# Kernel tuning notes

Measured on AMD Instinct MI355X. Metric: run time of the kernel, lower is better.

## Reference

```python
import jax, jax.numpy as jnp
import numpy as np

N = 1_048_576   # number of time samples (light-curve length)
M = 8           # number of quasisep Exp kernel terms (state dimension)
LOG2PI = float(np.log(2.0 * np.pi))


def setup_inputs() -> dict:
    key = jax.random.key(0)
    k1, k2, k3, k4, k5 = jax.random.split(key, 5)
    # unsorted-but-nearly-sorted timestamps; module argsorts internally
    t = jax.random.uniform(k1, (N,), dtype=jnp.float32) * (N / 10.0)
    y = jax.random.normal(k2, (N,), dtype=jnp.float32)
    yerr = 0.1 + 0.05 * jax.random.uniform(k3, (N,), dtype=jnp.float32)
    # interleaved [log_scale_j, log_sigma_j] for M Exp terms, as ravel_pytree would produce
    log_scale = jnp.log(10.0) + 0.5 * jax.random.normal(k4, (M,), dtype=jnp.float32)
    log_sigma = 0.3 * jax.random.normal(k5, (M,), dtype=jnp.float32)
    log_kernel_param = jnp.stack([log_scale, log_sigma], axis=1).reshape(-1)
    return {"t": t, "y": y, "yerr": yerr, "log_kernel_param": log_kernel_param}


def _kalman_log_prob(ts, ys, diag, scale, sigma):
    """GP log-likelihood for k(tau)=sum_j sigma_j^2 exp(-tau/scale_j) via Kalman filter.

    State: M independent OU components; observation h = ones(M); zero mean.
    """
    Pinf = sigma * sigma                                   # stationary variances [M]
    dt = jnp.concatenate([jnp.zeros((1,), ts.dtype), jnp.diff(ts)])  # [N]

    def step(carry, inp):
        m, P, ll = carry                                   # m:[M], P:[M,M]
        dtn, yn, dn = inp
        phi = jnp.exp(-dtn / scale)                        # transition diag [M]
        m_pred = phi * m
        # P_pred = Phi P Phi^T + Q,  Q = diag(Pinf*(1-phi^2))
        P_pred = (phi[:, None] * phi[None, :]) * P + jnp.diag(Pinf * (1.0 - phi * phi))
        Ph = P_pred.sum(axis=1)                            # P_pred @ h
        S = Ph.sum() + dn                                  # innovation variance
        v = yn - m_pred.sum()                              # innovation (zero mean)
        K = Ph / S                                         # Kalman gain
        m_new = m_pred + K * v
        P_new = P_pred - K[:, None] * Ph[None, :]
        ll_new = ll - 0.5 * (LOG2PI + jnp.log(S) + v * v / S)
        return (m_new, P_new, ll_new), None

    m0 = jnp.zeros((M,), ts.dtype)
    P0 = jnp.diag(Pinf)
    (_, _, ll), _ = jax.lax.scan(step, (m0, P0, jnp.zeros((), ts.dtype)), (dt, ys, diag))
    return ll


def reference(t, y, yerr, log_kernel_param):
    # UniVarModel.log_prob: sort by time, diag = yerr^2 (has_jitter=False),
    # kernel params exponentiated, zero mean.
    inds = jnp.argsort(t)
    ts, ys, diag = t[inds], y[inds], yerr[inds] ** 2
    p = jnp.exp(log_kernel_param)
    scale, sigma = p[0::2], p[1::2]
    return _kalman_log_prob(ts, ys, diag, scale, sigma)
```

## Files before the change

### kernel.cpp

```cpp
#include <hip/hip_runtime.h>
#include <stdint.h>

typedef unsigned long long u64;

#define CHUNK 64
#define WARM  8
#define SLEN  (WARM + CHUNK)
#define CPW   8
#define PD    8
#define NB    16384
#define NR    1024
#define BCAP  128
#define HBLK  64
#define LOG2PI_F 1.8378770664093453f

__device__ __forceinline__ int bucket_of(float tv, float scale) {
    int b = (int)(tv * scale);
    return b > (NB - 1) ? (NB - 1) : (b < 0 ? 0 : b);
}

__global__ __launch_bounds__(256) void hist_k(const float4* __restrict__ t4,
                                              unsigned* __restrict__ hp,
                                              float scale, int n4) {
    __shared__ unsigned lh[NR];
    for (int v = threadIdx.x; v < NR; v += 256) lh[v] = 0u;
    __syncthreads();
    for (int i = blockIdx.x * 256 + threadIdx.x; i < n4; i += gridDim.x * 256) {
        float4 tv = t4[i];
        atomicAdd(&lh[bucket_of(tv.x, scale) >> 4], 1u);
        atomicAdd(&lh[bucket_of(tv.y, scale) >> 4], 1u);
        atomicAdd(&lh[bucket_of(tv.z, scale) >> 4], 1u);
        atomicAdd(&lh[bucket_of(tv.w, scale) >> 4], 1u);
    }
    __syncthreads();
    for (int v = threadIdx.x; v < NR; v += 256)
        hp[blockIdx.x * NR + v] = lh[v];
}

__global__ __launch_bounds__(1024) void scan_k(const unsigned* __restrict__ hp,
                                               unsigned* __restrict__ roff,
                                               unsigned* __restrict__ rcnt) {
    __shared__ unsigned ws[16];
    const int r = threadIdx.x;
    unsigned tot = 0;
#pragma unroll 8
    for (int b = 0; b < HBLK; ++b) tot += hp[b * NR + r];
    unsigned s = tot;
#pragma unroll
    for (int d = 1; d < 64; d <<= 1) {
        unsigned v = __shfl_up(s, d);
        if ((r & 63) >= d) s += v;
    }
    if ((r & 63) == 63) ws[r >> 6] = s;
    __syncthreads();
    if (r < 16) {
        unsigned v = ws[r];
#pragma unroll
        for (int d = 1; d < 16; d <<= 1) {
            unsigned x = __shfl_up(v, d);
            if (r >= d) v += x;
        }
        ws[r] = v;
    }
    __syncthreads();
    unsigned wbase = (r >= 64) ? ws[(r >> 6) - 1] : 0u;
    unsigned excl = wbase + s - tot;
    roff[r] = excl; rcnt[r] = excl;
    if (r == NR - 1) roff[NR] = excl + tot;
}

__global__ __launch_bounds__(1024) void scatter1(const float4* __restrict__ t4,
                                                 unsigned* __restrict__ rcnt,
                                                 u64* __restrict__ keys1,
                                                 float scale) {
    __shared__ unsigned lh[NR], rb[NR];
    const int tid = threadIdx.x;
    lh[tid] = 0u;
    __syncthreads();
    const int i0 = blockIdx.x * 2048 + tid;
    float4 a = t4[i0], b = t4[i0 + 1024];
    float tv[8] = {a.x, a.y, a.z, a.w, b.x, b.y, b.z, b.w};
    unsigned id0 = 4u * (unsigned)i0, id1 = 4u * (unsigned)(i0 + 1024);
    unsigned ids[8] = {id0, id0 + 1, id0 + 2, id0 + 3,
                       id1, id1 + 1, id1 + 2, id1 + 3};
    int rr[8]; unsigned lp[8];
#pragma unroll
    for (int k = 0; k < 8; ++k) {
        rr[k] = bucket_of(tv[k], scale) >> 4;
        lp[k] = atomicAdd(&lh[rr[k]], 1u);
    }
    __syncthreads();
    {
        unsigned c = lh[tid];
        rb[tid] = c ? atomicAdd(&rcnt[tid], c) : 0u;
    }
    __syncthreads();
#pragma unroll
    for (int k = 0; k < 8; ++k) {
        unsigned bits = __float_as_uint(tv[k]);
        unsigned mk = (bits & 0x80000000u) ? ~bits : (bits | 0x80000000u);
        keys1[rb[rr[k]] + lp[k]] = ((u64)mk << 32) | (u64)ids[k];
    }
}

__device__ __forceinline__ float decode_key(unsigned h) {
    unsigned b = (h & 0x80000000u) ? (h ^ 0x80000000u) : ~h;
    return __uint_as_float(b);
}

__global__ __launch_bounds__(256) void sort_k(const u64* __restrict__ keys1,
                                              const unsigned* __restrict__ roff,
                                              float* __restrict__ tS,
                                              unsigned* __restrict__ idxS,
                                              float scale) {
    __shared__ u64 sk[16 * BCAP];
    __shared__ unsigned lh[16], pre[16];
    const int r = blockIdx.x;
    const int tid = threadIdx.x;
    for (int v = tid; v < 16 * BCAP; v += 256) sk[v] = ~0ull;
    if (tid < 16) lh[tid] = 0u;
    __syncthreads();
    const unsigned s = roff[r], e = roff[r + 1];
    for (unsigned u = s + tid; u < e; u += 256) {
        u64 kk = keys1[u];
        int b16 = bucket_of(decode_key((unsigned)(kk >> 32)), scale) & 15;
        unsigned lp = atomicAdd(&lh[b16], 1u);
        if (lp < (unsigned)BCAP) sk[b16 * BCAP + lp] = kk;
    }
    __syncthreads();
    if (tid == 0) {
        unsigned acc = 0;
#pragma unroll
        for (int c = 0; c < 16; ++c) {
            pre[c] = acc;
            unsigned cc = lh[c];
            acc += (cc > (unsigned)BCAP) ? (unsigned)BCAP : cc;
        }
    }
    for (int k = 2; k <= BCAP; k <<= 1) {
        for (int j = k >> 1; j >= 1; j >>= 1) {
#pragma unroll
            for (int it = 0; it < 4; ++it) {
                int w = it * 256 + tid;
                int q = w >> 6, p = w & 63;
                int i = ((p & ~(j - 1)) << 1) | (p & (j - 1));
                int si = q * BCAP + i, sp = si + j;
                bool up = ((i & k) == 0);
                u64 a = sk[si], bb = sk[sp];
                if ((a > bb) == up) { sk[si] = bb; sk[sp] = a; }
            }
            __syncthreads();
        }
    }
#pragma unroll
    for (int cp = 0; cp < 8; ++cp) {
        int c = cp * 2 + (tid >> 7);
        int el = tid & 127;
        unsigned cc = lh[c]; cc = (cc > (unsigned)BCAP) ? (unsigned)BCAP : cc;
        if (el < (int)cc) {
            u64 kk = sk[c * BCAP + el];
            unsigned pos = s + pre[c] + el;
            tS[pos] = decode_key((unsigned)(kk >> 32));
            idxS[pos] = (unsigned)kk;
        }
    }
}

__global__ __launch_bounds__(256) void gather_pay(const uint4* __restrict__ idx4,
                                                  const float* __restrict__ src,
                                                  float* __restrict__ dst,
                                                  int squared, int n8) {
    int i = blockIdx.x * 256 + threadIdx.x;
    if (i >= n8) return;
    uint4 a = idx4[2 * i], b = idx4[2 * i + 1];
    float4 o1, o2;
    o1.x = src[a.x]; o1.y = src[a.y]; o1.z = src[a.z]; o1.w = src[a.w];
    o2.x = src[b.x]; o2.y = src[b.y]; o2.z = src[b.z]; o2.w = src[b.w];
    if (squared) {
        o1.x *= o1.x; o1.y *= o1.y; o1.z *= o1.z; o1.w *= o1.w;
        o2.x *= o2.x; o2.y *= o2.y; o2.z *= o2.z; o2.w *= o2.w;
    }
    ((float4*)dst)[2 * i] = o1;
    ((float4*)dst)[2 * i + 1] = o2;
}

#define DPPMOV(x, ctrl) __int_as_float(__builtin_amdgcn_update_dpp( \
        0, __float_as_int(x), (ctrl), 0xF, 0xF, true))
#define GSUM8(s, x) { s = (x) + DPPMOV((x), 0xB1); s += DPPMOV(s, 0x4E); s += DPPMOV(s, 0x141); }
#define GATHER8(v, x) { \
    v[0] = (x); v[1] = DPPMOV((x), 0xB1); v[2] = DPPMOV((x), 0x4E); \
    v[3] = DPPMOV(v[1], 0x4E); v[7] = DPPMOV((x), 0x141); \
    v[6] = DPPMOV(v[1], 0x141); v[5] = DPPMOV(v[2], 0x141); v[4] = DPPMOV(v[3], 0x141); }

__global__ __launch_bounds__(64) void kalman8(
    const float* __restrict__ tS, const float* __restrict__ ysA,
    const float* __restrict__ dgA, const float* __restrict__ lkp,
    float* __restrict__ llp) {
    __shared__ float4 sty[SLEN * 8];
    const int lane = threadIdx.x & 63;
    const int g = lane >> 3, l = lane & 7;
    const int bi = blockIdx.x;
    const long base = (long)bi * (CPW * CHUNK) - WARM;

    const float INF = __builtin_huge_valf();
    const float t0 = tS[0];
#pragma unroll
    for (int gg = 0; gg < CPW; ++gg) {
        for (int v = lane; v < SLEN; v += 64) {
            long gi = base + gg * CHUNK + v;
            float tv, yv, dv;
            if (gi >= 0) { tv = tS[gi]; yv = ysA[gi]; dv = dgA[gi]; }
            else { tv = t0; yv = 0.0f; dv = INF; }
            sty[v * 8 + ((gg + v) & 7)] = make_float4(tv, yv, dv, 0.0f);
        }
    }
    long gp = base + g * CHUNK - 1;
    float stp = (gp >= 0) ? tS[gp] : t0;
    __syncthreads();

    const float L2E = 1.44269504088896340736f;
    const float LN2 = 0.6931471805599453f;
    const float c_own = -L2E * __expf(-lkp[2 * l]);
    const float Pinf  = __expf(2.0f * lkp[2 * l + 1]);

    float P[8];
    P[0] = Pinf;
#pragma unroll
    for (int k = 1; k < 8; ++k) P[k] = 0.0f;
    float m = 0.0f, llog = 0.0f, lvw = 0.0f;

#define KSTEP(LS, SCORED) { \
    const int slot_ = (LS) * 8 + ((g + (LS)) & 7); \
    float4 q4 = sty[slot_]; \
    float dtc = q4.x - stp; stp = q4.x; float yc = q4.y; float dc = q4.z; \
    float phi = __builtin_amdgcn_exp2f(dtc * c_own); \
    float fv[8]; GATHER8(fv, phi) \
    float q0 = phi * phi; \
    float dadd = fmaf(-q0, Pinf, Pinf); \
    float Pp[8]; \
    Pp[0] = fmaf(q0, P[0], dadd); \
    _Pragma("unroll") \
    for (int k = 1; k < 8; ++k) Pp[k] = (phi * fv[k]) * P[k]; \
    float Ph = ((Pp[0] + Pp[1]) + (Pp[2] + Pp[3])) + ((Pp[4] + Pp[5]) + (Pp[6] + Pp[7])); \
    float mp = phi * m; \
    float Ss; GSUM8(Ss, Ph) \
    float ms; GSUM8(ms, mp) \
    float S = Ss + dc; \
    float v = yc - ms; \
    float invS = __builtin_amdgcn_rcpf(S); \
    float w = v * invS; \
    float K = Ph * invS; \
    float pv[8]; GATHER8(pv, Ph) \
    _Pragma("unroll") \
    for (int k = 0; k < 8; ++k) P[k] = fmaf(-K, pv[k], Pp[k]); \
    m = fmaf(Ph, w, mp); \
    if (SCORED) { llog += __builtin_amdgcn_logf(S); lvw = fmaf(v, w, lvw); } }

    for (int ls = 0; ls < WARM; ls += PD) {
#pragma unroll
        for (int u = 0; u < PD; ++u) KSTEP(ls + u, false)
    }
    for (int ls = WARM; ls < SLEN; ls += PD) {
#pragma unroll
        for (int u = 0; u < PD; ++u) KSTEP(ls + u, true)
    }
#undef KSTEP

    if (l == 0)
        llp[bi * CPW + g] = -0.5f * (CHUNK * LOG2PI_F + LN2 * llog + lvw);
}

__global__ __launch_bounds__(256) void reduce_ll(const float* __restrict__ llp,
                                                 float* __restrict__ out, int g) {
    __shared__ float sred[4];
    int tid = threadIdx.x;
    float s = 0.0f;
    for (int i = tid; i < g; i += 256) s += llp[i];
    for (int m = 1; m < 64; m <<= 1) s += __shfl_xor(s, m);
    if ((tid & 63) == 0) sred[tid >> 6] = s;
    __syncthreads();
    if (tid == 0) out[0] = sred[0] + sred[1] + sred[2] + sred[3];
}

extern "C" void kernel_launch(void* const* d_in, const int* in_sizes, int n_in,
                              void* d_out, int out_size, void* d_ws, size_t ws_size,
                              hipStream_t stream) {
    const float* t    = (const float*)d_in[0];
    const float* y    = (const float*)d_in[1];
    const float* yerr = (const float*)d_in[2];
    const float* lkp  = (const float*)d_in[3];
    float* out = (float*)d_out;
    const int n = in_sizes[0];

    u64*      keys1 = (u64*)d_ws;
    float*    ysA   = (float*)d_ws;
    float*    dgA   = (float*)((char*)d_ws + (size_t)n * 4);
    float*    tS    = (float*)((char*)d_ws + (size_t)n * 8);
    unsigned* idxS  = (unsigned*)((char*)d_ws + (size_t)n * 12);
    float*    llp   = (float*)((char*)d_ws + (size_t)n * 16);
    unsigned* hp    = (unsigned*)(llp + 16384);
    unsigned* roff  = hp + HBLK * NR;
    unsigned* rcnt  = roff + NR + 64;

    const float scale = (float)NB / ((float)n / 10.0f);
    const int n4 = n / 4;
    const int n8 = n / 8;

    hist_k<<<HBLK, 256, 0, stream>>>((const float4*)t, hp, scale, n4);
    scan_k<<<1, 1024, 0, stream>>>(hp, roff, rcnt);
    scatter1<<<n4 / 2048, 1024, 0, stream>>>((const float4*)t, rcnt, keys1, scale);
    sort_k<<<NR, 256, 0, stream>>>(keys1, roff, tS, idxS, scale);
    gather_pay<<<(n8 + 255) / 256, 256, 0, stream>>>((const uint4*)idxS, y, ysA, 0, n8);
    gather_pay<<<(n8 + 255) / 256, 256, 0, stream>>>((const uint4*)idxS, yerr, dgA, 1, n8);

    const int G = n / CHUNK;
    kalman8<<<G / CPW, 64, 0, stream>>>(tS, ysA, dgA, lkp, llp);
    reduce_ll<<<1, 256, 0, stream>>>(llp, out, G);
}
```

Before: 111.2 us.

## Carry y and yerr^2 payload through bucket scatter and sort, drop gather kernels

The scatter pass now reads y and yerr alongside t and writes a packed (y, yerr^2) payload next to each key. Each key's low 11 bits hold a slot index local to its bucket. The sort kernel stages that payload in shared memory and writes sorted ys and diag directly, so the two random-access gather kernels and the idxS array go away. The risks are that the key's index field is truncated by the shift, and that buckets larger than 2048 entries would alias slots. The block also uses more shared memory.

New measurement: 106.0 us, median of 3. 4.7% less time.

```diff
diff --git a/kernel.cpp b/kernel.cpp
--- a/kernel.cpp
+++ b/kernel.cpp
@@ -11,6 +11,7 @@
 #define NB    16384
 #define NR    1024
 #define BCAP  128
+#define RCAP  2048
 #define HBLK  64
 #define LOG2PI_F 1.8378770664093453f
 
@@ -70,16 +71,24 @@
 }
 
 __global__ __launch_bounds__(1024) void scatter1(const float4* __restrict__ t4,
+                                                 const float4* __restrict__ y4,
+                                                 const float4* __restrict__ e4,
+                                                 const unsigned* __restrict__ roff,
                                                  unsigned* __restrict__ rcnt,
                                                  u64* __restrict__ keys1,
+                                                 float2* __restrict__ pay1,
                                                  float scale) {
-    __shared__ unsigned lh[NR], rb[NR];
+    __shared__ unsigned lh[NR], rb[NR], rloc[NR];
     const int tid = threadIdx.x;
     lh[tid] = 0u;
     __syncthreads();
     const int i0 = blockIdx.x * 2048 + tid;
     float4 a = t4[i0], b = t4[i0 + 1024];
+    float4 ya = y4[i0], yb = y4[i0 + 1024];
+    float4 ea = e4[i0], eb = e4[i0 + 1024];
     float tv[8] = {a.x, a.y, a.z, a.w, b.x, b.y, b.z, b.w};
+    float yv[8] = {ya.x, ya.y, ya.z, ya.w, yb.x, yb.y, yb.z, yb.w};
+    float ev[8] = {ea.x, ea.y, ea.z, ea.w, eb.x, eb.y, eb.z, eb.w};
     unsigned id0 = 4u * (unsigned)i0, id1 = 4u * (unsigned)(i0 + 1024);
     unsigned ids[8] = {id0, id0 + 1, id0 + 2, id0 + 3,
                        id1, id1 + 1, id1 + 2, id1 + 3};
@@ -92,14 +101,19 @@
     __syncthreads();
     {
         unsigned c = lh[tid];
-        rb[tid] = c ? atomicAdd(&rcnt[tid], c) : 0u;
+        unsigned base = c ? atomicAdd(&rcnt[tid], c) : 0u;
+        rb[tid] = base;
+        rloc[tid] = base - roff[tid];
     }
     __syncthreads();
 #pragma unroll
     for (int k = 0; k < 8; ++k) {
         unsigned bits = __float_as_uint(tv[k]);
         unsigned mk = (bits & 0x80000000u) ? ~bits : (bits | 0x80000000u);
-        keys1[rb[rr[k]] + lp[k]] = ((u64)mk << 32) | (u64)ids[k];
+        unsigned pos = rb[rr[k]] + lp[k];
+        unsigned slot = (rloc[rr[k]] + lp[k]) & 0x7FFu;
+        keys1[pos] = ((u64)mk << 32) | ((u64)(ids[k] << 11)) | (u64)slot;
+        pay1[pos] = make_float2(yv[k], ev[k] * ev[k]);
     }
 }
 
@@ -109,11 +123,14 @@
 }
 
 __global__ __launch_bounds__(256) void sort_k(const u64* __restrict__ keys1,
+                                              const float2* __restrict__ pay1,
                                               const unsigned* __restrict__ roff,
                                               float* __restrict__ tS,
-                                              unsigned* __restrict__ idxS,
+                                              float* __restrict__ ysA,
+                                              float* __restrict__ dgA,
                                               float scale) {
     __shared__ u64 sk[16 * BCAP];
+    __shared__ float2 sp[RCAP];
     __shared__ unsigned lh[16], pre[16];
     const int r = blockIdx.x;
     const int tid = threadIdx.x;
@@ -122,6 +139,7 @@
     __syncthreads();
     const unsigned s = roff[r], e = roff[r + 1];
     for (unsigned u = s + tid; u < e; u += 256) {
+        if (u - s < (unsigned)RCAP) sp[u - s] = pay1[u];
         u64 kk = keys1[u];
         int b16 = bucket_of(decode_key((unsigned)(kk >> 32)), scale) & 15;
         unsigned lp = atomicAdd(&lh[b16], 1u);
@@ -144,10 +162,10 @@
                 int w = it * 256 + tid;
                 int q = w >> 6, p = w & 63;
                 int i = ((p & ~(j - 1)) << 1) | (p & (j - 1));
-                int si = q * BCAP + i, sp = si + j;
+                int si = q * BCAP + i, sp_ = si + j;
                 bool up = ((i & k) == 0);
-                u64 a = sk[si], bb = sk[sp];
-                if ((a > bb) == up) { sk[si] = bb; sk[sp] = a; }
+                u64 a = sk[si], bb = sk[sp_];
+                if ((a > bb) == up) { sk[si] = bb; sk[sp_] = a; }
             }
             __syncthreads();
         }
@@ -160,28 +178,12 @@
         if (el < (int)cc) {
             u64 kk = sk[c * BCAP + el];
             unsigned pos = s + pre[c] + el;
+            float2 yd = sp[(unsigned)(kk & 0x7FFull)];
             tS[pos] = decode_key((unsigned)(kk >> 32));
-            idxS[pos] = (unsigned)kk;
-        }
-    }
-}
-
-__global__ __launch_bounds__(256) void gather_pay(const uint4* __restrict__ idx4,
-                                                  const float* __restrict__ src,
-                                                  float* __restrict__ dst,
-                                                  int squared, int n8) {
-    int i = blockIdx.x * 256 + threadIdx.x;
-    if (i >= n8) return;
-    uint4 a = idx4[2 * i], b = idx4[2 * i + 1];
-    float4 o1, o2;
-    o1.x = src[a.x]; o1.y = src[a.y]; o1.z = src[a.z]; o1.w = src[a.w];
-    o2.x = src[b.x]; o2.y = src[b.y]; o2.z = src[b.z]; o2.w = src[b.w];
-    if (squared) {
-        o1.x *= o1.x; o1.y *= o1.y; o1.z *= o1.z; o1.w *= o1.w;
-        o2.x *= o2.x; o2.y *= o2.y; o2.z *= o2.z; o2.w *= o2.w;
-    }
-    ((float4*)dst)[2 * i] = o1;
-    ((float4*)dst)[2 * i + 1] = o2;
+            ysA[pos] = yd.x;
+            dgA[pos] = yd.y;
+        }
+    }
 }
 
 #define DPPMOV(x, ctrl) __int_as_float(__builtin_amdgcn_update_dpp( \
@@ -293,25 +295,24 @@
     const int n = in_sizes[0];
 
     u64*      keys1 = (u64*)d_ws;
-    float*    ysA   = (float*)d_ws;
-    float*    dgA   = (float*)((char*)d_ws + (size_t)n * 4);
-    float*    tS    = (float*)((char*)d_ws + (size_t)n * 8);
-    unsigned* idxS  = (unsigned*)((char*)d_ws + (size_t)n * 12);
-    float*    llp   = (float*)((char*)d_ws + (size_t)n * 16);
+    float2*   pay1  = (float2*)((char*)d_ws + (size_t)n * 8);
+    float*    tS    = (float*)((char*)d_ws + (size_t)n * 16);
+    float*    ysA   = (float*)((char*)d_ws + (size_t)n * 20);
+    float*    dgA   = (float*)((char*)d_ws + (size_t)n * 24);
+    float*    llp   = (float*)((char*)d_ws + (size_t)n * 28);
     unsigned* hp    = (unsigned*)(llp + 16384);
     unsigned* roff  = hp + HBLK * NR;
     unsigned* rcnt  = roff + NR + 64;
 
     const float scale = (float)NB / ((float)n / 10.0f);
     const int n4 = n / 4;
-    const int n8 = n / 8;
 
     hist_k<<<HBLK, 256, 0, stream>>>((const float4*)t, hp, scale, n4);
     scan_k<<<1, 1024, 0, stream>>>(hp, roff, rcnt);
-    scatter1<<<n4 / 2048, 1024, 0, stream>>>((const float4*)t, rcnt, keys1, scale);
-    sort_k<<<NR, 256, 0, stream>>>(keys1, roff, tS, idxS, scale);
-    gather_pay<<<(n8 + 255) / 256, 256, 0, stream>>>((const uint4*)idxS, y, ysA, 0, n8);
-    gather_pay<<<(n8 + 255) / 256, 256, 0, stream>>>((const uint4*)idxS, yerr, dgA, 1, n8);
+    scatter1<<<n4 / 2048, 1024, 0, stream>>>((const float4*)t, (const float4*)y,
+                                             (const float4*)yerr, roff, rcnt,
+                                             keys1, pay1, scale);
+    sort_k<<<NR, 256, 0, stream>>>(keys1, pay1, roff, tS, ysA, dgA, scale);
 
     const int G = n / CHUNK;
     kalman8<<<G / CPW, 64, 0, stream>>>(tS, ysA, dgA, lkp, llp);
```
